# Kernel optimization log

Measured on AMD Instinct MI355X. Metric: run time of the kernel, lower is better.

The kernel has to match this reference:

```python
import jax, jax.numpy as jnp
import numpy as np

B, IN_DIM, OUT_DIM, HID, K, GH, NG = 512, 480, 400, 512, 8, 128, 32


def setup_inputs() -> dict:
    key = jax.random.key(0)
    ks = jax.random.split(key, 8)
    s = lambda fan: 1.0 / np.sqrt(fan)
    return {
        "x": jax.random.normal(ks[0], (B, IN_DIM), jnp.float32),
        "gating_idx": jnp.arange(NG, dtype=jnp.int64) + (IN_DIM - NG),
        "GW1": jax.random.normal(ks[1], (NG, GH), jnp.float32) * s(NG),
        "Gb1": jnp.zeros((GH,), jnp.float32),
        "GW2": jax.random.normal(ks[2], (GH, GH), jnp.float32) * s(GH),
        "Gb2": jnp.zeros((GH,), jnp.float32),
        "GW3": jax.random.normal(ks[3], (GH, K), jnp.float32) * s(GH),
        "Gb3": jnp.zeros((K,), jnp.float32),
        "Wk1": jax.random.normal(ks[4], (K, HID, IN_DIM), jnp.float32) * s(HID * IN_DIM) * 2.45,
        "bk1": jnp.zeros((K, HID), jnp.float32),
        "Wk2": jax.random.normal(ks[5], (K, HID, HID), jnp.float32) * s(HID * HID) * 2.45,
        "bk2": jnp.zeros((K, HID), jnp.float32),
        "Wk3": jax.random.normal(ks[6], (K, OUT_DIM, HID), jnp.float32) * s(OUT_DIM * HID) * 2.45,
        "bk3": jnp.zeros((K, OUT_DIM), jnp.float32),
    }


def _motion_layer(xin, g, Wk, bk):
    # blended per-sample weight: wi[b,o,i] = sum_k g[b,k] * Wk[k,o,i]
    # then per-sample matvec: out[b,o] = sum_i wi[b,o,i] * xin[b,i] + sum_k g[b,k]*bk[k,o]
    out = jnp.einsum('bk,koi,bi->bo', g, Wk, xin)
    return out + g @ bk


def reference(x, gating_idx, GW1, Gb1, GW2, Gb2, GW3, Gb3,
              Wk1, bk1, Wk2, bk2, Wk3, bk3):
    # gating MLP (elu, elu, linear)
    g_in = jnp.take(x, gating_idx, axis=-1)                 # [B, NG]
    h = jax.nn.elu(g_in @ GW1 + Gb1)
    h = jax.nn.elu(h @ GW2 + Gb2)
    g = h @ GW3 + Gb3                                       # [B, K] blend coefficients
    # motion network: 3 phase-blended expert layers
    y1 = jax.nn.elu(_motion_layer(x, g, Wk1, bk1))          # [B, HID]
    y2 = jax.nn.elu(_motion_layer(y1, g, Wk2, bk2))         # [B, HID]
    out = _motion_layer(y2, g, Wk3, bk3)                    # [B, OUT_DIM]
    return out
```

## Files before the change

kernel.cpp:

```cpp
#include <hip/hip_runtime.h>
#include <hip/hip_bf16.h>


typedef __hip_bfloat16 bf16;
typedef unsigned short u16;
typedef __attribute__((ext_vector_type(8))) short bf16x8;
typedef __attribute__((ext_vector_type(4))) float f32x4;

__device__ __forceinline__ float elu1(float x) { return x > 0.f ? x : expm1f(x); }

__device__ __forceinline__ u16 cvt1(float v) {
    union { bf16 h; u16 u; } c;
    c.h = __float2bfloat16(v);
    return c.u;
}

__device__ __forceinline__ void async16(const u16* g, u16* l) {
    __builtin_amdgcn_global_load_lds(
        (const __attribute__((address_space(1))) void*)g,
        (__attribute__((address_space(3))) void*)l, 16, 0, 0);
}

template <int NU>
__device__ __forceinline__ void cvt_units(const float* __restrict__ src,
                                          u16* __restrict__ dst, int b, int tid)
{
    #pragma unroll
    for (int jj = 0; jj < (NU + 255) / 256; ++jj) {
        const int local = jj * 256 + tid;
        if ((NU & 255) && local >= NU) break;
        const size_t off = ((size_t)b * NU + local) * 8;
        float4 a = *(const float4*)(src + off);
        float4 c = *(const float4*)(src + off + 4);
        union { u16 h[8]; uint4 v; } o;
        o.h[0] = cvt1(a.x); o.h[1] = cvt1(a.y); o.h[2] = cvt1(a.z); o.h[3] = cvt1(a.w);
        o.h[4] = cvt1(c.x); o.h[5] = cvt1(c.y); o.h[6] = cvt1(c.z); o.h[7] = cvt1(c.w);
        *(uint4*)(dst + off) = o.v;
    }
}

__global__ __launch_bounds__(256) void k_phase0(
    const float* __restrict__ x, const int* __restrict__ idx_raw,
    const float* __restrict__ GW1, const float* __restrict__ Gb1,
    const float* __restrict__ GW2, const float* __restrict__ Gb2,
    const float* __restrict__ GW3, const float* __restrict__ Gb3,
    const float* __restrict__ Wk1,
    float* __restrict__ gout, u16* __restrict__ xbf, u16* __restrict__ Wb1)
{
    __shared__ float xg[32];
    __shared__ float h1[128];
    __shared__ float h2[128];
    const int b = blockIdx.x;
    const int j = threadIdx.x;

    if (j < 32) {
        int ii;
        if (idx_raw[1] == 0) ii = (int)((const long long*)idx_raw)[j];
        else                 ii = idx_raw[j];
        if (ii < 0 || ii >= 480) ii = 448 + j;
        xg[j] = x[(size_t)b * 480 + ii];
    }
    __syncthreads();

    if (j < 128) {
        float a = Gb1[j];
        #pragma unroll
        for (int i = 0; i < 32; ++i) a += xg[i] * GW1[i * 128 + j];
        h1[j] = elu1(a);
    }
    __syncthreads();

    if (j < 128) {
        float a2 = Gb2[j];
        #pragma unroll 8
        for (int i = 0; i < 128; ++i) a2 += h1[i] * GW2[i * 128 + j];
        h2[j] = elu1(a2);
    }
    __syncthreads();

    if (j < 8) {
        float a3 = Gb3[j];
        for (int i = 0; i < 128; ++i) a3 += h2[i] * GW3[i * 8 + j];
        gout[b * 8 + j] = a3;
    }

    for (int i = j; i < 480; i += 256)
        xbf[b * 480 + i] = cvt1(x[b * 480 + i]);

    cvt_units<480>(Wk1, Wb1, b, j);
}

template <int IDIM, int ODIM, bool ELU, typename OutT>
__device__ __forceinline__ void layer_phase(
    const u16* __restrict__ A,
    const u16* __restrict__ Wb,
    const float* __restrict__ bk,
    const float* __restrict__ gv,
    OutT* __restrict__ out,
    u16* wbuf)
{
    constexpr int KW = 64;
    constexpr int NW = (IDIM + KW - 1) / KW;
    constexpr int NC = IDIM / 32;
    const int bid = blockIdx.x;
    const int o0 = (bid & 31) * 16;
    if (o0 >= ODIM) return;
    const int m0  = (bid >> 5) * 32;
    const int tid = threadIdx.x;
    const int wid = tid >> 6, lane = tid & 63;
    const int n = lane & 15, quad = lane >> 4;
    const int e0 = wid * 2;

    bf16x8 areg[2][NC];
    #pragma unroll
    for (int s = 0; s < 2; ++s)
        #pragma unroll
        for (int c = 0; c < NC; ++c)
            areg[s][c] = *(const bf16x8*)(A + (size_t)(m0 + 16 * s + n) * IDIM
                                            + c * 32 + quad * 8);

    auto stage = [&](int w, u16* buf) {
        const int w0 = w * KW;
        #pragma unroll
        for (int t = 0; t < 4; ++t) {
            const int L = (wid * 4 + t) * 64 + lane;
            const int r = L >> 3, slot = L & 7;
            const int e = r >> 4, nr = r & 15;
            int koff = w0 + (slot ^ (nr & 7)) * 8;
            if (koff + 8 > IDIM) koff = IDIM - 8;
            async16(Wb + ((size_t)(e * ODIM + o0 + nr)) * IDIM + koff,
                    buf + (size_t)(wid * 4 + t) * 512);
        }
    };

    const f32x4 zero = {0.f, 0.f, 0.f, 0.f};
    f32x4 acc[2][2] = {{zero, zero}, {zero, zero}};

    stage(0, wbuf);
    __syncthreads();

    #pragma unroll
    for (int w = 0; w < NW; ++w) {
        if (w + 1 < NW) stage(w + 1, wbuf + ((w + 1) & 1) * (128 * KW));
        const u16* buf = wbuf + (w & 1) * (128 * KW);
        #pragma unroll
        for (int cl = 0; cl < 2; ++cl) {
            const int c = w * 2 + cl;
            if (c >= NC) break;
            const int cw = cl * 4 + quad;
            const int sl = (cw ^ (n & 7)) * 8;
            #pragma unroll
            for (int jj = 0; jj < 2; ++jj) {
                bf16x8 bfr = *(const bf16x8*)(buf + ((e0 + jj) * 16 + n) * KW + sl);
                acc[0][jj] = __builtin_amdgcn_mfma_f32_16x16x32_bf16(areg[0][c], bfr, acc[0][jj], 0, 0, 0);
                acc[1][jj] = __builtin_amdgcn_mfma_f32_16x16x32_bf16(areg[1][c], bfr, acc[1][jj], 0, 0, 0);
            }
        }
        __syncthreads();
    }

    float* part = (float*)wbuf;
    float bkv[2];
    #pragma unroll
    for (int jj = 0; jj < 2; ++jj) bkv[jj] = bk[(e0 + jj) * ODIM + o0 + n];

    #pragma unroll
    for (int s = 0; s < 2; ++s) {
        #pragma unroll
        for (int r = 0; r < 4; ++r) {
            const int lrow = 16 * s + 4 * quad + r;
            const int grow = m0 + lrow;
            float v = 0.f;
            #pragma unroll
            for (int jj = 0; jj < 2; ++jj)
                v += gv[grow * 8 + e0 + jj] * (acc[s][jj][r] + bkv[jj]);
            part[(wid * 32 + lrow) * 17 + n] = v;
        }
    }
    __syncthreads();

    #pragma unroll
    for (int rr = 0; rr < 2; ++rr) {
        const int lrow = rr * 16 + (tid >> 4);
        const int col  = tid & 15;
        float v = part[lrow * 17 + col] + part[(32 + lrow) * 17 + col]
                + part[(64 + lrow) * 17 + col] + part[(96 + lrow) * 17 + col];
        if (ELU) v = elu1(v);
        if constexpr (__hip_internal::is_same<OutT, float>::value)
            out[(size_t)(m0 + lrow) * ODIM + o0 + col] = v;
        else
            out[(size_t)(m0 + lrow) * ODIM + o0 + col] = cvt1(v);
    }
}

template <int IDIM, int ODIM, bool ELU, typename OutT, int NU_NEXT>
__global__ __launch_bounds__(256, 2) void k_layer(
    const u16* __restrict__ A, const u16* __restrict__ Wb,
    const float* __restrict__ bk, const float* __restrict__ gv,
    OutT* __restrict__ out,
    const float* __restrict__ Wnext_src, u16* __restrict__ Wnext_dst)
{
    __shared__ u16 wbuf[2][128 * 64];
    layer_phase<IDIM, ODIM, ELU, OutT>(A, Wb, bk, gv, out, &wbuf[0][0]);
    if constexpr (NU_NEXT > 0)
        cvt_units<NU_NEXT>(Wnext_src, Wnext_dst, blockIdx.x, threadIdx.x);
}

extern "C" void kernel_launch(void* const* d_in, const int* in_sizes, int n_in,
                              void* d_out, int out_size, void* d_ws, size_t ws_size,
                              hipStream_t stream)
{
    const float* x   = (const float*)d_in[0];
    const int* gidx  = (const int*)d_in[1];
    const float* GW1 = (const float*)d_in[2];
    const float* Gb1 = (const float*)d_in[3];
    const float* GW2 = (const float*)d_in[4];
    const float* Gb2 = (const float*)d_in[5];
    const float* GW3 = (const float*)d_in[6];
    const float* Gb3 = (const float*)d_in[7];
    const float* Wk1 = (const float*)d_in[8];
    const float* bk1 = (const float*)d_in[9];
    const float* Wk2 = (const float*)d_in[10];
    const float* bk2 = (const float*)d_in[11];
    const float* Wk3 = (const float*)d_in[12];
    const float* bk3 = (const float*)d_in[13];

    char* ws  = (char*)d_ws;
    float* g  = (float*)ws;
    u16* xbf  = (u16*)(ws + (64 << 10));
    u16* A1   = (u16*)(ws + (1 << 20));
    u16* A2   = (u16*)(ws + (1 << 20) + (512 << 10));
    u16* Wb1  = (u16*)(ws + (2 << 20));
    u16* Wb2  = (u16*)(ws + (6 << 20));
    u16* Wb3  = (u16*)(ws + (10 << 20));

    k_phase0<<<512, 256, 0, stream>>>(x, gidx, GW1, Gb1, GW2, Gb2,
                                      GW3, Gb3, Wk1, g, xbf, Wb1);
    k_layer<480, 512, true,  u16,  512><<<512, 256, 0, stream>>>(
        xbf, Wb1, bk1, g, A1, Wk2, Wb2);
    k_layer<512, 512, true,  u16,  400><<<512, 256, 0, stream>>>(
        A1,  Wb2, bk2, g, A2, Wk3, Wb3);
    k_layer<512, 400, false, float, 0><<<512, 256, 0, stream>>>(
        A2,  Wb3, bk3, g, (float*)d_out, (const float*)nullptr, (u16*)nullptr);
}
```

Before: 139.8 us.

## Fuse fp32-to-bf16 weight conversion into layer kernels' register-staged pipeline

Drops the separate pass that converted the expert weights and input x to bf16 in workspace. Each layer kernel now loads fp32 weights straight from global memory into registers, converts them, and writes bf16 into the swizzled LDS double buffer, prefetching two windows ahead. The A operand is also loaded per chunk, and converted from fp32 for layer 1, instead of being preloaded into registers. This removes the bf16 workspace writes and re-reads but doubles the weight bytes each block reads, and it adds register pressure and conversion ALU work inside the main loop.

```diff
diff --git a/kernel.cpp b/kernel.cpp
--- a/kernel.cpp
+++ b/kernel.cpp
@@ -15,37 +15,12 @@
     return c.u;
 }
 
-__device__ __forceinline__ void async16(const u16* g, u16* l) {
-    __builtin_amdgcn_global_load_lds(
-        (const __attribute__((address_space(1))) void*)g,
-        (__attribute__((address_space(3))) void*)l, 16, 0, 0);
-}
-
-template <int NU>
-__device__ __forceinline__ void cvt_units(const float* __restrict__ src,
-                                          u16* __restrict__ dst, int b, int tid)
-{
-    #pragma unroll
-    for (int jj = 0; jj < (NU + 255) / 256; ++jj) {
-        const int local = jj * 256 + tid;
-        if ((NU & 255) && local >= NU) break;
-        const size_t off = ((size_t)b * NU + local) * 8;
-        float4 a = *(const float4*)(src + off);
-        float4 c = *(const float4*)(src + off + 4);
-        union { u16 h[8]; uint4 v; } o;
-        o.h[0] = cvt1(a.x); o.h[1] = cvt1(a.y); o.h[2] = cvt1(a.z); o.h[3] = cvt1(a.w);
-        o.h[4] = cvt1(c.x); o.h[5] = cvt1(c.y); o.h[6] = cvt1(c.z); o.h[7] = cvt1(c.w);
-        *(uint4*)(dst + off) = o.v;
-    }
-}
-
-__global__ __launch_bounds__(256) void k_phase0(
+__global__ __launch_bounds__(256) void k_gating(
     const float* __restrict__ x, const int* __restrict__ idx_raw,
     const float* __restrict__ GW1, const float* __restrict__ Gb1,
     const float* __restrict__ GW2, const float* __restrict__ Gb2,
     const float* __restrict__ GW3, const float* __restrict__ Gb3,
-    const float* __restrict__ Wk1,
-    float* __restrict__ gout, u16* __restrict__ xbf, u16* __restrict__ Wb1)
+    float* __restrict__ gout)
 {
     __shared__ float xg[32];
     __shared__ float h1[128];
@@ -83,25 +58,19 @@
         for (int i = 0; i < 128; ++i) a3 += h2[i] * GW3[i * 8 + j];
         gout[b * 8 + j] = a3;
     }
-
-    for (int i = j; i < 480; i += 256)
-        xbf[b * 480 + i] = cvt1(x[b * 480 + i]);
-
-    cvt_units<480>(Wk1, Wb1, b, j);
-}
-
-template <int IDIM, int ODIM, bool ELU, typename OutT>
-__device__ __forceinline__ void layer_phase(
-    const u16* __restrict__ A,
-    const u16* __restrict__ Wb,
+}
+
+template <int IDIM, int ODIM, bool ELU, bool AF32, typename OutT>
+__global__ __launch_bounds__(256, 2) void k_layer(
+    const void* __restrict__ Aptr,
+    const float* __restrict__ Wf,
     const float* __restrict__ bk,
     const float* __restrict__ gv,
-    OutT* __restrict__ out,
-    u16* wbuf)
+    OutT* __restrict__ out)
 {
     constexpr int KW = 64;
     constexpr int NW = (IDIM + KW - 1) / KW;
-    constexpr int NC = IDIM / 32;
+    __shared__ u16 wbuf[2][128 * KW];
     const int bid = blockIdx.x;
     const int o0 = (bid & 31) * 16;
     if (o0 >= ODIM) return;
@@ -111,55 +80,87 @@
     const int n = lane & 15, quad = lane >> 4;
     const int e0 = wid * 2;
 
-    bf16x8 areg[2][NC];
-    #pragma unroll
-    for (int s = 0; s < 2; ++s)
-        #pragma unroll
-        for (int c = 0; c < NC; ++c)
-            areg[s][c] = *(const bf16x8*)(A + (size_t)(m0 + 16 * s + n) * IDIM
-                                            + c * 32 + quad * 8);
-
-    auto stage = [&](int w, u16* buf) {
-        const int w0 = w * KW;
-        #pragma unroll
-        for (int t = 0; t < 4; ++t) {
-            const int L = (wid * 4 + t) * 64 + lane;
-            const int r = L >> 3, slot = L & 7;
-            const int e = r >> 4, nr = r & 15;
-            int koff = w0 + (slot ^ (nr & 7)) * 8;
+    size_t rowoff[4]; int coff[4];
+    #pragma unroll
+    for (int q = 0; q < 4; ++q) {
+        const int L = q * 256 + tid;
+        const int r = L >> 3, c8 = L & 7;
+        const int e = r >> 4, nr = r & 15;
+        rowoff[q] = (size_t)(e * ODIM + o0 + nr) * IDIM;
+        coff[q]   = (c8 ^ (nr & 7)) * 8;
+    }
+    auto issue = [&](int w, float4 (&f)[4][2]) {
+        #pragma unroll
+        for (int q = 0; q < 4; ++q) {
+            int koff = w * KW + coff[q];
             if (koff + 8 > IDIM) koff = IDIM - 8;
-            async16(Wb + ((size_t)(e * ODIM + o0 + nr)) * IDIM + koff,
-                    buf + (size_t)(wid * 4 + t) * 512);
+            const float* p = Wf + rowoff[q] + koff;
+            f[q][0] = *(const float4*)p;
+            f[q][1] = *(const float4*)(p + 4);
+        }
+    };
+    auto commit = [&](float4 (&f)[4][2], u16* buf) {
+        #pragma unroll
+        for (int q = 0; q < 4; ++q) {
+            union { u16 h[8]; uint4 v; } o;
+            o.h[0] = cvt1(f[q][0].x); o.h[1] = cvt1(f[q][0].y);
+            o.h[2] = cvt1(f[q][0].z); o.h[3] = cvt1(f[q][0].w);
+            o.h[4] = cvt1(f[q][1].x); o.h[5] = cvt1(f[q][1].y);
+            o.h[6] = cvt1(f[q][1].z); o.h[7] = cvt1(f[q][1].w);
+            *(uint4*)(buf + (size_t)(q * 256 + tid) * 8) = o.v;
         }
     };
 
     const f32x4 zero = {0.f, 0.f, 0.f, 0.f};
     f32x4 acc[2][2] = {{zero, zero}, {zero, zero}};
-
-    stage(0, wbuf);
+    float4 fa[4][2], fb[4][2];
+
+    issue(0, fa);
+    commit(fa, wbuf[0]);
+    issue(1, fb);
     __syncthreads();
 
     #pragma unroll
     for (int w = 0; w < NW; ++w) {
-        if (w + 1 < NW) stage(w + 1, wbuf + ((w + 1) & 1) * (128 * KW));
-        const u16* buf = wbuf + (w & 1) * (128 * KW);
+        u16* cur = wbuf[w & 1];
+        u16* nxt = wbuf[(w + 1) & 1];
+        if (w + 1 < NW) { if (w & 1) commit(fa, nxt); else commit(fb, nxt); }
+        if (w + 2 < NW) { if (w & 1) issue(w + 2, fb); else issue(w + 2, fa); }
         #pragma unroll
         for (int cl = 0; cl < 2; ++cl) {
-            const int c = w * 2 + cl;
-            if (c >= NC) break;
-            const int cw = cl * 4 + quad;
-            const int sl = (cw ^ (n & 7)) * 8;
+            const int i0 = w * KW + cl * 32;
+            if (i0 >= IDIM) break;
+            bf16x8 af[2];
+            #pragma unroll
+            for (int s = 0; s < 2; ++s) {
+                if constexpr (AF32) {
+                    const float* ap = (const float*)Aptr
+                        + (size_t)(m0 + 16 * s + n) * IDIM + i0 + quad * 8;
+                    float4 u = *(const float4*)ap;
+                    float4 v = *(const float4*)(ap + 4);
+                    union { u16 h[8]; bf16x8 b; } t;
+                    t.h[0] = cvt1(u.x); t.h[1] = cvt1(u.y);
+                    t.h[2] = cvt1(u.z); t.h[3] = cvt1(u.w);
+                    t.h[4] = cvt1(v.x); t.h[5] = cvt1(v.y);
+                    t.h[6] = cvt1(v.z); t.h[7] = cvt1(v.w);
+                    af[s] = t.b;
+                } else {
+                    af[s] = *(const bf16x8*)((const u16*)Aptr
+                        + (size_t)(m0 + 16 * s + n) * IDIM + i0 + quad * 8);
+                }
+            }
+            const int sl = ((cl * 4 + quad) ^ (n & 7)) * 8;
             #pragma unroll
             for (int jj = 0; jj < 2; ++jj) {
-                bf16x8 bfr = *(const bf16x8*)(buf + ((e0 + jj) * 16 + n) * KW + sl);
-                acc[0][jj] = __builtin_amdgcn_mfma_f32_16x16x32_bf16(areg[0][c], bfr, acc[0][jj], 0, 0, 0);
-                acc[1][jj] = __builtin_amdgcn_mfma_f32_16x16x32_bf16(areg[1][c], bfr, acc[1][jj], 0, 0, 0);
+                bf16x8 bfr = *(const bf16x8*)(cur + ((e0 + jj) * 16 + n) * KW + sl);
+                acc[0][jj] = __builtin_amdgcn_mfma_f32_16x16x32_bf16(af[0], bfr, acc[0][jj], 0, 0, 0);
+                acc[1][jj] = __builtin_amdgcn_mfma_f32_16x16x32_bf16(af[1], bfr, acc[1][jj], 0, 0, 0);
             }
         }
         __syncthreads();
     }
 
-    float* part = (float*)wbuf;
+    float* part = (float*)&wbuf[0][0];
     float bkv[2];
     #pragma unroll
     for (int jj = 0; jj < 2; ++jj) bkv[jj] = bk[(e0 + jj) * ODIM + o0 + n];
@@ -191,19 +192,6 @@
         else
             out[(size_t)(m0 + lrow) * ODIM + o0 + col] = cvt1(v);
     }
-}
-
-template <int IDIM, int ODIM, bool ELU, typename OutT, int NU_NEXT>
-__global__ __launch_bounds__(256, 2) void k_layer(
-    const u16* __restrict__ A, const u16* __restrict__ Wb,
-    const float* __restrict__ bk, const float* __restrict__ gv,
-    OutT* __restrict__ out,
-    const float* __restrict__ Wnext_src, u16* __restrict__ Wnext_dst)
-{
-    __shared__ u16 wbuf[2][128 * 64];
-    layer_phase<IDIM, ODIM, ELU, OutT>(A, Wb, bk, gv, out, &wbuf[0][0]);
-    if constexpr (NU_NEXT > 0)
-        cvt_units<NU_NEXT>(Wnext_src, Wnext_dst, blockIdx.x, threadIdx.x);
 }
 
 extern "C" void kernel_launch(void* const* d_in, const int* in_sizes, int n_in,
@@ -227,19 +215,15 @@
 
     char* ws  = (char*)d_ws;
     float* g  = (float*)ws;
-    u16* xbf  = (u16*)(ws + (64 << 10));
     u16* A1   = (u16*)(ws + (1 << 20));
     u16* A2   = (u16*)(ws + (1 << 20) + (512 << 10));
-    u16* Wb1  = (u16*)(ws + (2 << 20));
-    u16* Wb2  = (u16*)(ws + (6 << 20));
-    u16* Wb3  = (u16*)(ws + (10 << 20));
-
-    k_phase0<<<512, 256, 0, stream>>>(x, gidx, GW1, Gb1, GW2, Gb2,
-                                      GW3, Gb3, Wk1, g, xbf, Wb1);
-    k_layer<480, 512, true,  u16,  512><<<512, 256, 0, stream>>>(
-        xbf, Wb1, bk1, g, A1, Wk2, Wb2);
-    k_layer<512, 512, true,  u16,  400><<<512, 256, 0, stream>>>(
-        A1,  Wb2, bk2, g, A2, Wk3, Wb3);
-    k_layer<512, 400, false, float, 0><<<512, 256, 0, stream>>>(
-        A2,  Wb3, bk3, g, (float*)d_out, (const float*)nullptr, (u16*)nullptr);
-}
+
+    k_gating<<<512, 256, 0, stream>>>(x, gidx, GW1, Gb1, GW2, Gb2,
+                                      GW3, Gb3, g);
+    k_layer<480, 512, true,  true,  u16> <<<512, 256, 0, stream>>>(
+        x,  Wk1, bk1, g, A1);
+    k_layer<512, 512, true,  false, u16> <<<512, 256, 0, stream>>>(
+        A1, Wk2, bk2, g, A2);
+    k_layer<512, 400, false, false, float><<<512, 256, 0, stream>>>(
+        A2, Wk3, bk3, g, (float*)d_out);
+}
```

Measured after the change: 148.7 us. 1.06x slower.
